# Kernel tuning notes

Measured on AMD Instinct MI355X. Metric: run time of the kernel, lower is better.

The kernel has to match this reference:

```python
import jax, jax.numpy as jnp
import numpy as np

B, S, CACHE, HID, NH, NKV, HD, INTER = 2, 1024, 2048, 2048, 8, 1, 256, 16384
EPS = 1e-6
SOFTCAP = 50.0
SCALE = HD ** -0.5  # query_pre_attn_scalar is None -> head_dim**-0.5
NEG = -1e9


def _rms(x, w, eps=EPS):
    # Gemma RMSNorm: fp32 norm, output scaled by (1 + weight)
    x32 = x.astype(jnp.float32)
    n = x32 * jax.lax.rsqrt(jnp.mean(x32 * x32, axis=-1, keepdims=True) + eps)
    return (n * (1.0 + w)).astype(x.dtype)


def _rope(x, cos, sin):
    # half-split complex rotation (Gemma apply_rotary_emb): first half real, second half imag
    d2 = x.shape[-1] // 2
    x1, x2 = x[..., :d2], x[..., d2:]
    c = cos[None, :, None, :]
    s = sin[None, :, None, :]
    return jnp.concatenate([x1 * c - x2 * s, x1 * s + x2 * c], axis=-1).astype(x.dtype)


def setup_inputs() -> dict:
    key = jax.random.key(0)
    ks = jax.random.split(key, 8)
    sc = lambda k, sh, f: jax.random.normal(k, sh, jnp.float32) * f
    inp = {}
    inp["hidden_states"] = sc(ks[0], (B, S, HID), 1.0)
    inv = 1.0 / (10000.0 ** (np.arange(0, HD, 2, dtype=np.float32) / HD))
    t = np.arange(S, dtype=np.float32)[:, None] * inv[None, :]
    inp["cos"] = jnp.asarray(np.cos(t), jnp.float32)
    inp["sin"] = jnp.asarray(np.sin(t), jnp.float32)
    inp["kv_write_indices"] = jnp.arange(S, dtype=jnp.int32)
    inp["k_cache"] = jnp.zeros((B, CACHE, NKV, HD), jnp.float32)
    inp["v_cache"] = jnp.zeros((B, CACHE, NKV, HD), jnp.float32)
    i = jnp.arange(S)[:, None]
    j = jnp.arange(CACHE)[None, :]
    inp["mask"] = jnp.where(j <= i, 0.0, NEG).astype(jnp.float32)[None, None]  # [1,1,S,CACHE]
    inp["w_qkv"] = sc(ks[1], ((NH + 2 * NKV) * HD, HID), 0.02)
    inp["w_o"] = sc(ks[2], (HID, NH * HD), 0.02)
    inp["w_gate"] = sc(ks[3], (INTER, HID), 0.02)
    inp["w_up"] = sc(ks[4], (INTER, HID), 0.02)
    inp["w_down"] = sc(ks[5], (HID, INTER), 0.02)
    inp["ln_in"] = jnp.zeros((HID,), jnp.float32)
    inp["ln_post"] = jnp.zeros((HID,), jnp.float32)
    inp["q_norm"] = jnp.zeros((HD,), jnp.float32)
    inp["k_norm"] = jnp.zeros((HD,), jnp.float32)
    return inp


def reference(hidden_states, cos, sin, kv_write_indices, k_cache, v_cache, mask,
              w_qkv, w_o, w_gate, w_up, w_down, ln_in, ln_post, q_norm, k_norm):
    # ---- attention sub-block ----
    res = hidden_states
    x = _rms(hidden_states, ln_in)
    qkv = x @ w_qkv.T  # [B,S,(NH+2*NKV)*HD]
    xq, xk, xv = jnp.split(qkv, [NH * HD, NH * HD + NKV * HD], axis=-1)
    xq = xq.reshape(B, S, NH, HD)
    xk = xk.reshape(B, S, NKV, HD)
    xv = xv.reshape(B, S, NKV, HD)
    xq = _rms(xq, q_norm)  # QK-norm
    xk = _rms(xk, k_norm)
    xq = _rope(xq, cos, sin)
    xk = _rope(xk, cos, sin)
    # KV-cache write (index_copy_ on dim 1)
    k_cache = k_cache.at[:, kv_write_indices].set(xk)
    v_cache = v_cache.at[:, kv_write_indices].set(xv)
    key = jnp.repeat(k_cache, NH // NKV, axis=2)  # [B,CACHE,NH,HD]
    val = jnp.repeat(v_cache, NH // NKV, axis=2)
    scores = jnp.einsum('bshd,bthd->bhst', xq * SCALE, key)  # [B,NH,S,CACHE]
    scores = jnp.tanh(scores / SOFTCAP) * SOFTCAP            # logit softcapping
    probs = jax.nn.softmax(scores + mask, axis=-1)
    out = jnp.einsum('bhst,bthd->bshd', probs, val).reshape(B, S, NH * HD)
    h = res + out @ w_o.T
    # ---- MLP sub-block ----
    res = h
    x = _rms(h, ln_post)
    gate = jax.nn.gelu(x @ w_gate.T, approximate=True)
    up = x @ w_up.T
    return res + (gate * up) @ w_down.T
```

## Files before the change

kernel.cpp:

```cpp
#include <hip/hip_runtime.h>
#include <hip/hip_bf16.h>

typedef __attribute__((ext_vector_type(8))) short short8;
typedef __attribute__((ext_vector_type(4))) float f32x4;
typedef unsigned short u16;

#define B_N 2
#define S_N 1024
#define HID_N 2048
#define NH_N 8
#define HD_N 256
#define INTER_N 16384

#define GLB(p) ((const __attribute__((address_space(1))) void*)(p))
#define AS3(p) ((__attribute__((address_space(3))) void*)(p))

__device__ inline u16 f2b_rn(float f) {
    union { float f; unsigned int u; } x; x.f = f;
    unsigned int r = x.u + 0x7fffu + ((x.u >> 16) & 1u);
    return (u16)(r >> 16);
}
__device__ inline float b2f(u16 h) {
    union { unsigned int u; float f; } x; x.u = ((unsigned int)h) << 16;
    return x.f;
}
__device__ inline float gelu_fast(float v) {
    float z = 0.7978845608028654f * (v + 0.044715f * v * v * v);
    float e = exp2f(z * 2.8853900817779268f);
    float th = 1.f - 2.f * __builtin_amdgcn_rcpf(e + 1.f);
    return 0.5f * v * (1.f + th);
}

__global__ __launch_bounds__(256) void convert_f2b(const float* __restrict__ in,
                                                   u16* __restrict__ out, int n4) {
    int i = blockIdx.x * 256 + threadIdx.x;
    int stride = gridDim.x * 256;
    for (; i < n4; i += stride) {
        float4 v = reinterpret_cast<const float4*>(in)[i];
        u16 o[4] = { f2b_rn(v.x), f2b_rn(v.y), f2b_rn(v.z), f2b_rn(v.w) };
        reinterpret_cast<ulonglong1*>(out)[i] = *reinterpret_cast<ulonglong1*>(o);
    }
}

__global__ __launch_bounds__(256) void convert_gu(const float* __restrict__ wg,
                                                  const float* __restrict__ wu,
                                                  u16* __restrict__ out, int n4) {
    int i = blockIdx.x * 256 + threadIdx.x;
    int stride = gridDim.x * 256;
    for (; i < n4; i += stride) {
        const int e = i << 2;
        const int r = e >> 11, c = e & 2047;
        const int rg = ((r >> 7) << 8) + (r & 127);
        float4 g = reinterpret_cast<const float4*>(wg)[i];
        u16 og[4] = { f2b_rn(g.x), f2b_rn(g.y), f2b_rn(g.z), f2b_rn(g.w) };
        *reinterpret_cast<ulonglong1*>(out + (size_t)rg * 2048 + c) =
            *reinterpret_cast<ulonglong1*>(og);
        float4 u = reinterpret_cast<const float4*>(wu)[i];
        u16 ou[4] = { f2b_rn(u.x), f2b_rn(u.y), f2b_rn(u.z), f2b_rn(u.w) };
        *reinterpret_cast<ulonglong1*>(out + (size_t)(rg + 128) * 2048 + c) =
            *reinterpret_cast<ulonglong1*>(ou);
    }
}

__global__ __launch_bounds__(256) void rmsnorm_k(const float* __restrict__ x,
                                                 const float* __restrict__ w,
                                                 u16* __restrict__ out) {
    const int row = blockIdx.x;
    const int tid = threadIdx.x;
    const float* xr = x + (size_t)row * HID_N;
    const float4* xr4 = reinterpret_cast<const float4*>(xr);
    float4 a = xr4[tid * 2], b = xr4[tid * 2 + 1];
    float s = a.x*a.x + a.y*a.y + a.z*a.z + a.w*a.w
            + b.x*b.x + b.y*b.y + b.z*b.z + b.w*b.w;
    for (int off = 32; off > 0; off >>= 1) s += __shfl_xor(s, off, 64);
    __shared__ float red[4];
    if ((tid & 63) == 0) red[tid >> 6] = s;
    __syncthreads();
    float tot = red[0] + red[1] + red[2] + red[3];
    float inv = rsqrtf(tot * (1.0f / HID_N) + 1e-6f);
    const float4* w4 = reinterpret_cast<const float4*>(w);
    float4 wa = w4[tid * 2], wb = w4[tid * 2 + 1];
    short8 o;
    o[0] = (short)f2b_rn(a.x * inv * (1.f + wa.x));
    o[1] = (short)f2b_rn(a.y * inv * (1.f + wa.y));
    o[2] = (short)f2b_rn(a.z * inv * (1.f + wa.z));
    o[3] = (short)f2b_rn(a.w * inv * (1.f + wa.w));
    o[4] = (short)f2b_rn(b.x * inv * (1.f + wb.x));
    o[5] = (short)f2b_rn(b.y * inv * (1.f + wb.y));
    o[6] = (short)f2b_rn(b.z * inv * (1.f + wb.z));
    o[7] = (short)f2b_rn(b.w * inv * (1.f + wb.w));
    reinterpret_cast<short8*>(out + (size_t)row * HID_N)[tid] = o;
}

__global__ __launch_bounds__(256) void qkv_post_k(const float* __restrict__ qkv,
                                                  const float* __restrict__ cosb,
                                                  const float* __restrict__ sinb,
                                                  const int* __restrict__ kvw,
                                                  const float* __restrict__ qn,
                                                  const float* __restrict__ kn,
                                                  u16* __restrict__ qb,
                                                  u16* __restrict__ kb,
                                                  u16* __restrict__ vt) {
    const int bs = blockIdx.x, vi = blockIdx.y;
    const int b = bs >> 10, s = bs & 1023;
    const int tid = threadIdx.x;
    const float* row = qkv + (size_t)bs * 2560;
    const int sdst = kvw[s];
    if (vi == 9) {
        vt[((size_t)(b * 256 + tid)) * 1024 + sdst] = f2b_rn(row[2304 + tid]);
        return;
    }
    __shared__ float buf[256];
    __shared__ float red[4];
    float val = row[vi * 256 + tid];
    float ss = val * val;
    for (int off = 32; off > 0; off >>= 1) ss += __shfl_xor(ss, off, 64);
    if ((tid & 63) == 0) red[tid >> 6] = ss;
    __syncthreads();
    float ms = (red[0] + red[1] + red[2] + red[3]) * (1.f / 256.f) + 1e-6f;
    const float* nw = (vi < 8) ? qn : kn;
    float nrm = val * rsqrtf(ms) * (1.f + nw[tid]);
    buf[tid] = nrm;
    __syncthreads();
    const float cv = cosb[s * 128 + (tid & 127)];
    const float sv = sinb[s * 128 + (tid & 127)];
    float o;
    if (tid < 128) o = buf[tid] * cv - buf[tid + 128] * sv;
    else           o = buf[tid - 128] * sv + buf[tid] * cv;
    if (vi < 8) qb[(((size_t)(b * 8 + vi)) * 1024 + s) * 256 + tid] = f2b_rn(o * 0.0625f);
    else        kb[((size_t)(b * 1024 + sdst)) * 256 + tid] = f2b_rn(o);
}

__global__ __launch_bounds__(256) void attn_k(const u16* __restrict__ qb,
                                              const u16* __restrict__ kb,
                                              const u16* __restrict__ vt,
                                              float* __restrict__ po,
                                              float* __restrict__ pl) {
    const int qt = blockIdx.x;
    const int h  = blockIdx.y;
    const int c  = blockIdx.z >> 1;
    const int b  = blockIdx.z & 1;
    if (qt < 4 * c) return;
    const int tid = threadIdx.x, lane = tid & 63, wid = tid >> 6;
    const int g = lane >> 4, li = lane & 15;
    const int q0 = qt * 64 + wid * 16;
    const int kv_lo = c * 256;
    __shared__ u16 pbuf[4][16 * 32];

    short8 qf[8];
    const size_t qbase = (((size_t)(b * 8 + h)) * 1024 + q0 + li) * 256;
    #pragma unroll
    for (int kk = 0; kk < 8; ++kk)
        qf[kk] = *reinterpret_cast<const short8*>(qb + qbase + kk * 32 + g * 8);

    f32x4 o[16], o1;
    #pragma unroll
    for (int d = 0; d < 16; ++d) o[d] = f32x4{0.f, 0.f, 0.f, 0.f};
    o1 = f32x4{0.f, 0.f, 0.f, 0.f};
    short8 onesf;
    #pragma unroll
    for (int j = 0; j < 8; ++j) onesf[j] = (short)0x3F80;

    const int nt = (min(kv_lo + 256, q0 + 16) - kv_lo + 31) >> 5;
    const int prd = li * 32 + ((g * 8) ^ (((li >> 2) & 3) * 8));

    for (int t = 0; t < nt; ++t) {
        const int kv0 = kv_lo + t * 32;
        f32x4 sc[2];
        sc[0] = f32x4{0.f, 0.f, 0.f, 0.f};
        sc[1] = f32x4{0.f, 0.f, 0.f, 0.f};
        #pragma unroll
        for (int ch = 0; ch < 2; ++ch) {
            const size_t kbase = ((size_t)(b * 1024 + kv0 + ch * 16 + li)) * 256;
            #pragma unroll
            for (int kk = 0; kk < 8; ++kk) {
                short8 kf = *reinterpret_cast<const short8*>(kb + kbase + kk * 32 + g * 8);
                sc[ch] = __builtin_amdgcn_mfma_f32_16x16x32_bf16(qf[kk], kf, sc[ch], 0, 0, 0);
            }
        }
        #pragma unroll
        for (int reg = 0; reg < 4; ++reg) {
            const int qrow = q0 + g * 4 + reg;
            const int prow = g * 4 + reg;
            const int pswz = ((prow >> 2) & 3) * 8;
            #pragma unroll
            for (int ch = 0; ch < 2; ++ch) {
                const int col = kv0 + ch * 16 + li;
                float s = sc[ch][reg];
                float e = exp2f(s * 0.05770780163555854f);
                float th = 1.f - 2.f * __builtin_amdgcn_rcpf(e + 1.f);
                float pv = exp2f(th * 72.13475204444817f);
                pv = (col <= qrow) ? pv : 0.f;
                pbuf[wid][prow * 32 + ((ch * 16 + li) ^ pswz)] = f2b_rn(pv);
            }
        }
        short8 pf = *reinterpret_cast<const short8*>(&pbuf[wid][prd]);
        o1 = __builtin_amdgcn_mfma_f32_16x16x32_bf16(pf, onesf, o1, 0, 0, 0);
        #pragma unroll
        for (int dth = 0; dth < 2; ++dth) {
            short8 vf[8];
            #pragma unroll
            for (int d8 = 0; d8 < 8; ++d8) {
                const int dt = dth * 8 + d8;
                vf[d8] = *reinterpret_cast<const short8*>(
                    vt + ((size_t)(b * 256 + dt * 16 + li)) * 1024 + kv0 + g * 8);
            }
            #pragma unroll
            for (int d8 = 0; d8 < 8; ++d8)
                o[dth * 8 + d8] = __builtin_amdgcn_mfma_f32_16x16x32_bf16(pf, vf[d8], o[dth * 8 + d8], 0, 0, 0);
        }
    }
    const size_t pbase = ((size_t)((c * 2 + b) * 8 + h)) * 1024;
    #pragma unroll
    for (int reg = 0; reg < 4; ++reg) {
        const int row = q0 + g * 4 + reg;
        #pragma unroll
        for (int dt = 0; dt < 16; ++dt)
            po[(pbase + row) * 256 + dt * 16 + li] = o[dt][reg];
        if (li == 0) pl[pbase + row] = o1[reg];
    }
}

__global__ __launch_bounds__(256) void attn_red_k(const float* __restrict__ po,
                                                  const float* __restrict__ pl,
                                                  u16* __restrict__ out) {
    const int gid = blockIdx.x;
    const int b = gid >> 10, s = gid & 1023;
    const int tid = threadIdx.x;
    const int h = tid >> 5, d0 = (tid & 31) * 8;
    const int cmax = s >> 8;
    float l = 0.f;
    float4 a0 = float4{0.f, 0.f, 0.f, 0.f}, a1 = float4{0.f, 0.f, 0.f, 0.f};
    for (int ci = 0; ci <= cmax; ++ci) {
        const size_t r = ((size_t)((ci * 2 + b) * 8 + h)) * 1024 + s;
        l += pl[r];
        float4 b0 = *reinterpret_cast<const float4*>(po + r * 256 + d0);
        float4 b1 = *reinterpret_cast<const float4*>(po + r * 256 + d0 + 4);
        a0.x += b0.x; a0.y += b0.y; a0.z += b0.z; a0.w += b0.w;
        a1.x += b1.x; a1.y += b1.y; a1.z += b1.z; a1.w += b1.w;
    }
    const float inv = 1.f / l;
    u16 r[8] = { f2b_rn(a0.x * inv), f2b_rn(a0.y * inv), f2b_rn(a0.z * inv), f2b_rn(a0.w * inv),
                 f2b_rn(a1.x * inv), f2b_rn(a1.y * inv), f2b_rn(a1.z * inv), f2b_rn(a1.w * inv) };
    *reinterpret_cast<ulonglong2*>(out + ((size_t)gid) * 2048 + h * 256 + d0) =
        *reinterpret_cast<ulonglong2*>(r);
}

template <int EPI>
__global__ __launch_bounds__(256) void gemm_bt(const u16* __restrict__ A,
                                               const u16* __restrict__ W,
                                               const float* __restrict__ res,
                                               float* __restrict__ outf,
                                               int M, int N, int K) {
    __shared__ u16 As[2][128 * 64];
    __shared__ u16 Bs[2][128 * 64];
    const int tid = threadIdx.x, lane = tid & 63, wid = tid >> 6;
    const int g = lane >> 4, li = lane & 15;
    const int wr = wid >> 1, wc = wid & 1;
    const int m0 = blockIdx.x * 128, n0 = blockIdx.y * 128;

    f32x4 acc[4][4];
    #pragma unroll
    for (int m = 0; m < 4; ++m)
        #pragma unroll
        for (int n = 0; n < 4; ++n) acc[m][n] = f32x4{0.f, 0.f, 0.f, 0.f};

    const int lrow = lane >> 3;
    const int lcol = (lane & 7) ^ lrow;
    const u16* ga0 = A + (size_t)(m0 + wid * 32 + lrow) * K + lcol * 8;
    const u16* gb0 = W + (size_t)(n0 + wid * 32 + lrow) * K + lcol * 8;
    const int lbase = wid * 32 * 64;

    auto STAGE = [&](int buf, int k0) {
        #pragma unroll
        for (int i = 0; i < 4; ++i) {
            __builtin_amdgcn_global_load_lds(GLB(ga0 + k0 + (size_t)(i * 8) * K),
                                             AS3(&As[buf][lbase + i * 8 * 64]), 16, 0, 0);
            __builtin_amdgcn_global_load_lds(GLB(gb0 + k0 + (size_t)(i * 8) * K),
                                             AS3(&Bs[buf][lbase + i * 8 * 64]), 16, 0, 0);
        }
    };

    const int NT = K >> 6;
    STAGE(0, 0);
    int cur = 0;
    for (int t = 0; t < NT; ++t) {
        if (t + 1 < NT) {
            STAGE(cur ^ 1, (t + 1) << 6);
            asm volatile("s_waitcnt vmcnt(8)" ::: "memory");
        } else {
            asm volatile("s_waitcnt vmcnt(0)" ::: "memory");
        }
        __builtin_amdgcn_s_barrier();
        __builtin_amdgcn_sched_barrier(0);
        #pragma unroll
        for (int kh = 0; kh < 2; ++kh) {
            short8 af[4], bfr[4];
            #pragma unroll
            for (int m = 0; m < 4; ++m) {
                int rw = wr * 64 + m * 16 + li;
                int slot = (kh * 4 + g) ^ (rw & 7);
                af[m] = *reinterpret_cast<const short8*>(&As[cur][rw * 64 + slot * 8]);
            }
            #pragma unroll
            for (int n = 0; n < 4; ++n) {
                int rw = wc * 64 + n * 16 + li;
                int slot = (kh * 4 + g) ^ (rw & 7);
                bfr[n] = *reinterpret_cast<const short8*>(&Bs[cur][rw * 64 + slot * 8]);
            }
            #pragma unroll
            for (int m = 0; m < 4; ++m)
                #pragma unroll
                for (int n = 0; n < 4; ++n)
                    acc[m][n] = __builtin_amdgcn_mfma_f32_16x16x32_bf16(af[m], bfr[n], acc[m][n], 0, 0, 0);
        }
        __builtin_amdgcn_s_barrier();
        cur ^= 1;
    }

    #pragma unroll
    for (int m = 0; m < 4; ++m) {
        #pragma unroll
        for (int n = 0; n < 4; ++n) {
            #pragma unroll
            for (int reg = 0; reg < 4; ++reg) {
                int row = m0 + wr * 64 + m * 16 + g * 4 + reg;
                int col = n0 + wc * 64 + n * 16 + li;
                size_t idx = (size_t)row * N + col;
                float v = acc[m][n][reg];
                if (EPI == 0) outf[idx] = v;
                else          outf[idx] = v + res[idx];
            }
        }
    }
}

template <int EPI>
__global__ __launch_bounds__(512, 2) void gemm256(const u16* __restrict__ A,
                                                  const u16* __restrict__ W,
                                                  float* __restrict__ outf,
                                                  u16* __restrict__ outb,
                                                  int M, int N, int K, int kcN) {
    __shared__ u16 Als[2][256 * 64];
    __shared__ u16 Bls[2][256 * 64];
    const int tid = threadIdx.x, lane = tid & 63, wid = tid >> 6;
    const int g = lane >> 4, li = lane & 15;
    const int wm = wid >> 2, wn = wid & 3;
    const int m0 = blockIdx.y * 256, n0 = blockIdx.x * 256;

    int koff = 0, Keff = K;
    if (EPI == 4) {
        Keff = K / kcN;
        koff = blockIdx.z * Keff;
        outf += (size_t)blockIdx.z * M * N;
    }

    f32x4 acc[8][4];
    #pragma unroll
    for (int m = 0; m < 8; ++m)
        #pragma unroll
        for (int n = 0; n < 4; ++n) acc[m][n] = f32x4{0.f, 0.f, 0.f, 0.f};

    const int srcg = ((tid & 7) ^ ((tid >> 3) & 7)) * 8;
    const u16* Asrc = A + (size_t)(m0 + (tid >> 3)) * K + koff + srcg;
    const u16* Bsrc = W + (size_t)(n0 + (tid >> 3)) * K + koff + srcg;
    const int dstb = wid * 512;

    auto STAGE_A = [&](int bf, int h, int kt) {
        const int k0 = kt << 6;
        #pragma unroll
        for (int i = 0; i < 2; ++i)
            __builtin_amdgcn_global_load_lds(GLB(Asrc + (size_t)(h * 128 + i * 64) * K + k0),
                                             AS3(&Als[bf][h * 8192 + i * 4096 + dstb]), 16, 0, 0);
    };
    auto STAGE_B = [&](int bf, int h, int kt) {
        const int k0 = kt << 6;
        #pragma unroll
        for (int i = 0; i < 2; ++i)
            __builtin_amdgcn_global_load_lds(GLB(Bsrc + (size_t)(h * 128 + i * 64) * K + k0),
                                             AS3(&Bls[bf][h * 8192 + i * 4096 + dstb]), 16, 0, 0);
    };
    auto LDA = [&](short8* d, int mh, int cb) {
        #pragma unroll
        for (int m = 0; m < 4; ++m) {
            const int rw = mh * 128 + wm * 64 + m * 16 + li;
            #pragma unroll
            for (int kh = 0; kh < 2; ++kh) {
                const int slot = (kh * 4 + g) ^ (rw & 7);
                d[m * 2 + kh] = *reinterpret_cast<const short8*>(&Als[cb][rw * 64 + slot * 8]);
            }
        }
    };
    auto LDB = [&](short8* d, int nh, int cb) {
        #pragma unroll
        for (int n = 0; n < 2; ++n) {
            const int rw = nh * 128 + wn * 32 + n * 16 + li;
            #pragma unroll
            for (int kh = 0; kh < 2; ++kh) {
                const int slot = (kh * 4 + g) ^ (rw & 7);
                d[n * 2 + kh] = *reinterpret_cast<const short8*>(&Bls[cb][rw * 64 + slot * 8]);
            }
        }
    };

    short8 af[8], af2[8], bq0[4], bq1[4];
    auto MQ = [&](int mh, int nh, short8* aa, short8* bb) {
        #pragma unroll
        for (int kh = 0; kh < 2; ++kh)
            #pragma unroll
            for (int m = 0; m < 4; ++m)
                #pragma unroll
                for (int n = 0; n < 2; ++n)
                    acc[mh * 4 + m][nh * 2 + n] = __builtin_amdgcn_mfma_f32_16x16x32_bf16(
                        aa[m * 2 + kh], bb[n * 2 + kh], acc[mh * 4 + m][nh * 2 + n], 0, 0, 0);
    };

    const int NT = Keff >> 6;
    STAGE_A(0, 0, 0); STAGE_B(0, 0, 0); STAGE_B(0, 1, 0); STAGE_A(0, 1, 0);
    {
        const int t1 = (1 < NT) ? 1 : NT - 1;
        STAGE_A(1, 0, t1); STAGE_B(1, 0, t1); STAGE_B(1, 1, t1);
    }
    asm volatile("s_waitcnt vmcnt(6)" ::: "memory");
    __builtin_amdgcn_s_barrier();
    __builtin_amdgcn_sched_barrier(0);
    LDA(af2, 0, 0);

    int cur = 0;
    for (int t = 0; t < NT; ++t) {
        const int tp1 = (t + 1 < NT) ? t + 1 : NT - 1;
        const int tp2 = (t + 2 < NT) ? t + 2 : NT - 1;
        LDB(bq0, 0, cur);
        STAGE_A(cur ^ 1, 1, tp1);
        __builtin_amdgcn_s_barrier();
        __builtin_amdgcn_s_setprio(1);
        MQ(0, 0, af2, bq0);
        __builtin_amdgcn_s_setprio(0);
        __builtin_amdgcn_s_barrier();
        LDB(bq1, 1, cur);
        STAGE_A(cur, 0, tp2);
        __builtin_amdgcn_s_barrier();
        __builtin_amdgcn_s_setprio(1);
        MQ(0, 1, af2, bq1);
        __builtin_amdgcn_s_setprio(0);
        __builtin_amdgcn_s_barrier();
        LDA(af, 1, cur);
        STAGE_B(cur, 0, tp2);
        __builtin_amdgcn_s_barrier();
        __builtin_amdgcn_s_setprio(1);
        MQ(1, 1, af, bq1);
        __builtin_amdgcn_s_setprio(0);
        __builtin_amdgcn_s_barrier();
        STAGE_B(cur, 1, tp2);
        __builtin_amdgcn_s_setprio(1);
        MQ(1, 0, af, bq0);
        __builtin_amdgcn_s_setprio(0);
        asm volatile("s_waitcnt vmcnt(6)" ::: "memory");
        __builtin_amdgcn_s_barrier();
        __builtin_amdgcn_sched_barrier(0);
        LDA(af2, 0, cur ^ 1);
        cur ^= 1;
    }

    if (EPI == 5) {
        #pragma unroll
        for (int mg = 0; mg < 8; ++mg) {
            const int mh = mg >> 2, m = mg & 3;
            #pragma unroll
            for (int n = 0; n < 2; ++n) {
                const int col = (n0 >> 1) + wn * 32 + n * 16 + li;
                #pragma unroll
                for (int reg = 0; reg < 4; ++reg) {
                    const int row = m0 + mh * 128 + wm * 64 + m * 16 + g * 4 + reg;
                    float gt = gelu_fast(acc[mg][n][reg]);
                    float up = acc[mg][n + 2][reg];
                    outb[(size_t)row * INTER_N + col] = f2b_rn(gt * up);
                }
            }
        }
    } else {
        #pragma unroll
        for (int mg = 0; mg < 8; ++mg) {
            const int mh = mg >> 2, m = mg & 3;
            #pragma unroll
            for (int ng = 0; ng < 4; ++ng) {
                const int nh = ng >> 1, n = ng & 1;
                #pragma unroll
                for (int reg = 0; reg < 4; ++reg) {
                    const int row = m0 + mh * 128 + wm * 64 + m * 16 + g * 4 + reg;
                    const int col = n0 + nh * 128 + wn * 32 + n * 16 + li;
                    outf[(size_t)row * N + col] = acc[mg][ng][reg];
                }
            }
        }
    }
}

__global__ __launch_bounds__(256) void reduce4_k(const float* __restrict__ part,
                                                 const float* __restrict__ res,
                                                 float* __restrict__ out, int n4) {
    int i = blockIdx.x * 256 + threadIdx.x;
    int stride = gridDim.x * 256;
    const size_t ps = (size_t)HID_N * B_N * S_N / 4;
    const float4* p4 = reinterpret_cast<const float4*>(part);
    const float4* r4 = reinterpret_cast<const float4*>(res);
    float4* o4 = reinterpret_cast<float4*>(out);
    for (; i < n4; i += stride) {
        float4 a = p4[i], b = p4[i + ps], c = p4[i + 2 * ps], d = p4[i + 3 * ps];
        float4 r = r4[i];
        float4 o;
        o.x = r.x + a.x + b.x + c.x + d.x;
        o.y = r.y + a.y + b.y + c.y + d.y;
        o.z = r.z + a.z + b.z + c.z + d.z;
        o.w = r.w + a.w + b.w + c.w + d.w;
        o4[i] = o;
    }
}

extern "C" void kernel_launch(void* const* d_in, const int* in_sizes, int n_in,
                              void* d_out, int out_size, void* d_ws, size_t ws_size,
                              hipStream_t stream) {
    (void)in_sizes; (void)n_in; (void)out_size; (void)ws_size;
    const float* hs     = (const float*)d_in[0];
    const float* cosb   = (const float*)d_in[1];
    const float* sinb   = (const float*)d_in[2];
    const int*   kvw    = (const int*)d_in[3];
    const float* wqkv   = (const float*)d_in[7];
    const float* wo     = (const float*)d_in[8];
    const float* wg     = (const float*)d_in[9];
    const float* wu     = (const float*)d_in[10];
    const float* wd     = (const float*)d_in[11];
    const float* ln_in  = (const float*)d_in[12];
    const float* ln_post= (const float*)d_in[13];
    const float* qn     = (const float*)d_in[14];
    const float* kn     = (const float*)d_in[15];
    float* out = (float*)d_out;

    char* p = (char*)d_ws;
    auto alloc = [&](size_t bytes) {
        char* r = p;
        p += (bytes + 255) & ~(size_t)255;
        return r;
    };
    u16* wqkv_b = (u16*)alloc(2560ull * 2048 * 2);
    u16* wo_b   = (u16*)alloc(2048ull * 2048 * 2);
    u16* wgu_b  = (u16*)alloc(32768ull * 2048 * 2);
    u16* wd_b   = (u16*)alloc(2048ull * 16384 * 2);
    u16* xn     = (u16*)alloc(2048ull * 2048 * 2);
    float* qkvf = (float*)alloc(2048ull * 2560 * 4);
    u16* qbuf   = (u16*)alloc(2ull * 8 * 1024 * 256 * 2);
    u16* kbuf   = (u16*)alloc(2ull * 1024 * 256 * 2);
    u16* vtbuf  = (u16*)alloc(2ull * 256 * 1024 * 2);
    u16* attn_o = (u16*)alloc(2048ull * 2048 * 2);
    float* hbuf = (float*)alloc(2048ull * 2048 * 4);
    u16* x2     = (u16*)alloc(2048ull * 2048 * 2);
    u16* actb   = (u16*)alloc(2048ull * 16384 * 2);
    float* po   = (float*)alloc(8ull * 8 * 1024 * 256 * 4);
    float* plse = (float*)alloc(8ull * 8 * 1024 * 4);
    float* partials = (float*)d_ws;

    auto conv = [&](const float* src, u16* dst, long n) {
        int n4 = (int)(n / 4);
        long blk = (n4 + 255) / 256;
        if (blk > 4096) blk = 4096;
        convert_f2b<<<dim3((unsigned)blk), dim3(256), 0, stream>>>(src, dst, n4);
    };
    conv(wqkv, wqkv_b, 2560l * 2048);
    conv(wo,   wo_b,   2048l * 2048);
    convert_gu<<<dim3(4096), dim3(256), 0, stream>>>(wg, wu, wgu_b, 8388608);
    conv(wd,   wd_b,   2048l * 16384);

    rmsnorm_k<<<dim3(2048), dim3(256), 0, stream>>>(hs, ln_in, xn);
    gemm_bt<0><<<dim3(16, 20), dim3(256), 0, stream>>>(xn, wqkv_b, nullptr,
                                                       qkvf, 2048, 2560, 2048);
    qkv_post_k<<<dim3(2048, 10), dim3(256), 0, stream>>>(qkvf, cosb, sinb, kvw, qn, kn,
                                                         qbuf, kbuf, vtbuf);
    attn_k<<<dim3(16, 8, 8), dim3(256), 0, stream>>>(qbuf, kbuf, vtbuf, po, plse);
    attn_red_k<<<dim3(2048), dim3(256), 0, stream>>>(po, plse, attn_o);
    gemm_bt<1><<<dim3(16, 16), dim3(256), 0, stream>>>(attn_o, wo_b, hs,
                                                       hbuf, 2048, 2048, 2048);
    rmsnorm_k<<<dim3(2048), dim3(256), 0, stream>>>(hbuf, ln_post, x2);
    gemm256<5><<<dim3(128, 8), dim3(512), 0, stream>>>(x2, wgu_b, nullptr, actb,
                                                       2048, 16384, 2048, 1);
    gemm256<4><<<dim3(8, 8, 4), dim3(512), 0, stream>>>(actb, wd_b, partials, nullptr,
                                                        2048, 2048, 16384, 4);
    reduce4_k<<<dim3(2048), dim3(256), 0, stream>>>(partials, hbuf, out, 1048576);
}
```

Before: 899.3 us.

## Rewrite 256x256 MLP GEMM to 1024-thread blocks with simple double buffering

The 256x256 GEMM used for the gate/up and down projections now runs with 16 waves per block instead of 8. Each wave owns a 64x64 output sub-tile with 16 accumulators instead of 32. The staged half-tile pipeline with setprio and interleaved LDS loads is replaced by a plain double-buffered loop: prefetch the next K-tile, wait, barrier, then compute. The gate/up weight interleave is changed to 32-row groups to match the new per-wave column split in the GELU epilogue. The aim is to cut register pressure and raise the wave count, at the cost of less careful overlap between memory and MFMA work and only one block per CU.

Measured after the change: 811.2 us, median of 3. 1.11x faster.

```diff
diff --git a/kernel.cpp b/kernel.cpp
--- a/kernel.cpp
+++ b/kernel.cpp
@@ -50,14 +50,14 @@
     for (; i < n4; i += stride) {
         const int e = i << 2;
         const int r = e >> 11, c = e & 2047;
-        const int rg = ((r >> 7) << 8) + (r & 127);
+        const int rg = ((r >> 5) << 6) + (r & 31);
         float4 g = reinterpret_cast<const float4*>(wg)[i];
         u16 og[4] = { f2b_rn(g.x), f2b_rn(g.y), f2b_rn(g.z), f2b_rn(g.w) };
         *reinterpret_cast<ulonglong1*>(out + (size_t)rg * 2048 + c) =
             *reinterpret_cast<ulonglong1*>(og);
         float4 u = reinterpret_cast<const float4*>(wu)[i];
         u16 ou[4] = { f2b_rn(u.x), f2b_rn(u.y), f2b_rn(u.z), f2b_rn(u.w) };
-        *reinterpret_cast<ulonglong1*>(out + (size_t)(rg + 128) * 2048 + c) =
+        *reinterpret_cast<ulonglong1*>(out + (size_t)(rg + 32) * 2048 + c) =
             *reinterpret_cast<ulonglong1*>(ou);
     }
 }
@@ -336,11 +336,11 @@
 }
 
 template <int EPI>
-__global__ __launch_bounds__(512, 2) void gemm256(const u16* __restrict__ A,
-                                                  const u16* __restrict__ W,
-                                                  float* __restrict__ outf,
-                                                  u16* __restrict__ outb,
-                                                  int M, int N, int K, int kcN) {
+__global__ __launch_bounds__(1024) void gemm256(const u16* __restrict__ A,
+                                                const u16* __restrict__ W,
+                                                float* __restrict__ outf,
+                                                u16* __restrict__ outb,
+                                                int M, int N, int K, int kcN) {
     __shared__ u16 Als[2][256 * 64];
     __shared__ u16 Bls[2][256 * 64];
     const int tid = threadIdx.x, lane = tid & 63, wid = tid >> 6;
@@ -355,141 +355,91 @@
         outf += (size_t)blockIdx.z * M * N;
     }
 
-    f32x4 acc[8][4];
-    #pragma unroll
-    for (int m = 0; m < 8; ++m)
+    f32x4 acc[4][4];
+    #pragma unroll
+    for (int m = 0; m < 4; ++m)
         #pragma unroll
         for (int n = 0; n < 4; ++n) acc[m][n] = f32x4{0.f, 0.f, 0.f, 0.f};
 
-    const int srcg = ((tid & 7) ^ ((tid >> 3) & 7)) * 8;
-    const u16* Asrc = A + (size_t)(m0 + (tid >> 3)) * K + koff + srcg;
-    const u16* Bsrc = W + (size_t)(n0 + (tid >> 3)) * K + koff + srcg;
+    const int trow = tid >> 3;
+    const int sgr = ((tid & 7) ^ (trow & 7)) * 8;
+    const u16* Asrc = A + (size_t)(m0 + trow) * K + koff + sgr;
+    const u16* Bsrc = W + (size_t)(n0 + trow) * K + koff + sgr;
     const int dstb = wid * 512;
 
-    auto STAGE_A = [&](int bf, int h, int kt) {
+    auto STAGE = [&](int bf, int kt) {
         const int k0 = kt << 6;
         #pragma unroll
-        for (int i = 0; i < 2; ++i)
-            __builtin_amdgcn_global_load_lds(GLB(Asrc + (size_t)(h * 128 + i * 64) * K + k0),
-                                             AS3(&Als[bf][h * 8192 + i * 4096 + dstb]), 16, 0, 0);
+        for (int i = 0; i < 2; ++i) {
+            __builtin_amdgcn_global_load_lds(GLB(Asrc + (size_t)(i * 128) * K + k0),
+                                             AS3(&Als[bf][i * 8192 + dstb]), 16, 0, 0);
+            __builtin_amdgcn_global_load_lds(GLB(Bsrc + (size_t)(i * 128) * K + k0),
+                                             AS3(&Bls[bf][i * 8192 + dstb]), 16, 0, 0);
+        }
     };
-    auto STAGE_B = [&](int bf, int h, int kt) {
-        const int k0 = kt << 6;
-        #pragma unroll
-        for (int i = 0; i < 2; ++i)
-            __builtin_amdgcn_global_load_lds(GLB(Bsrc + (size_t)(h * 128 + i * 64) * K + k0),
-                                             AS3(&Bls[bf][h * 8192 + i * 4096 + dstb]), 16, 0, 0);
-    };
-    auto LDA = [&](short8* d, int mh, int cb) {
-        #pragma unroll
-        for (int m = 0; m < 4; ++m) {
-            const int rw = mh * 128 + wm * 64 + m * 16 + li;
-            #pragma unroll
-            for (int kh = 0; kh < 2; ++kh) {
+
+    const int NT = Keff >> 6;
+    STAGE(0, 0);
+    int cur = 0;
+    for (int t = 0; t < NT; ++t) {
+        if (t + 1 < NT) {
+            STAGE(cur ^ 1, t + 1);
+            asm volatile("s_waitcnt vmcnt(4)" ::: "memory");
+        } else {
+            asm volatile("s_waitcnt vmcnt(0)" ::: "memory");
+        }
+        __builtin_amdgcn_s_barrier();
+        __builtin_amdgcn_sched_barrier(0);
+        #pragma unroll
+        for (int kh = 0; kh < 2; ++kh) {
+            short8 af[4], bfr[4];
+            #pragma unroll
+            for (int m = 0; m < 4; ++m) {
+                const int rw = wm * 64 + m * 16 + li;
                 const int slot = (kh * 4 + g) ^ (rw & 7);
-                d[m * 2 + kh] = *reinterpret_cast<const short8*>(&Als[cb][rw * 64 + slot * 8]);
-            }
-        }
-    };
-    auto LDB = [&](short8* d, int nh, int cb) {
-        #pragma unroll
-        for (int n = 0; n < 2; ++n) {
-            const int rw = nh * 128 + wn * 32 + n * 16 + li;
-            #pragma unroll
-            for (int kh = 0; kh < 2; ++kh) {
+                af[m] = *reinterpret_cast<const short8*>(&Als[cur][rw * 64 + slot * 8]);
+            }
+            #pragma unroll
+            for (int n = 0; n < 4; ++n) {
+                const int rw = wn * 64 + n * 16 + li;
                 const int slot = (kh * 4 + g) ^ (rw & 7);
-                d[n * 2 + kh] = *reinterpret_cast<const short8*>(&Bls[cb][rw * 64 + slot * 8]);
-            }
-        }
-    };
-
-    short8 af[8], af2[8], bq0[4], bq1[4];
-    auto MQ = [&](int mh, int nh, short8* aa, short8* bb) {
-        #pragma unroll
-        for (int kh = 0; kh < 2; ++kh)
+                bfr[n] = *reinterpret_cast<const short8*>(&Bls[cur][rw * 64 + slot * 8]);
+            }
             #pragma unroll
             for (int m = 0; m < 4; ++m)
                 #pragma unroll
-                for (int n = 0; n < 2; ++n)
-                    acc[mh * 4 + m][nh * 2 + n] = __builtin_amdgcn_mfma_f32_16x16x32_bf16(
-                        aa[m * 2 + kh], bb[n * 2 + kh], acc[mh * 4 + m][nh * 2 + n], 0, 0, 0);
-    };
-
-    const int NT = Keff >> 6;
-    STAGE_A(0, 0, 0); STAGE_B(0, 0, 0); STAGE_B(0, 1, 0); STAGE_A(0, 1, 0);
-    {
-        const int t1 = (1 < NT) ? 1 : NT - 1;
-        STAGE_A(1, 0, t1); STAGE_B(1, 0, t1); STAGE_B(1, 1, t1);
-    }
-    asm volatile("s_waitcnt vmcnt(6)" ::: "memory");
-    __builtin_amdgcn_s_barrier();
-    __builtin_amdgcn_sched_barrier(0);
-    LDA(af2, 0, 0);
-
-    int cur = 0;
-    for (int t = 0; t < NT; ++t) {
-        const int tp1 = (t + 1 < NT) ? t + 1 : NT - 1;
-        const int tp2 = (t + 2 < NT) ? t + 2 : NT - 1;
-        LDB(bq0, 0, cur);
-        STAGE_A(cur ^ 1, 1, tp1);
+                for (int n = 0; n < 4; ++n)
+                    acc[m][n] = __builtin_amdgcn_mfma_f32_16x16x32_bf16(af[m], bfr[n], acc[m][n], 0, 0, 0);
+        }
         __builtin_amdgcn_s_barrier();
-        __builtin_amdgcn_s_setprio(1);
-        MQ(0, 0, af2, bq0);
-        __builtin_amdgcn_s_setprio(0);
-        __builtin_amdgcn_s_barrier();
-        LDB(bq1, 1, cur);
-        STAGE_A(cur, 0, tp2);
-        __builtin_amdgcn_s_barrier();
-        __builtin_amdgcn_s_setprio(1);
-        MQ(0, 1, af2, bq1);
-        __builtin_amdgcn_s_setprio(0);
-        __builtin_amdgcn_s_barrier();
-        LDA(af, 1, cur);
-        STAGE_B(cur, 0, tp2);
-        __builtin_amdgcn_s_barrier();
-        __builtin_amdgcn_s_setprio(1);
-        MQ(1, 1, af, bq1);
-        __builtin_amdgcn_s_setprio(0);
-        __builtin_amdgcn_s_barrier();
-        STAGE_B(cur, 1, tp2);
-        __builtin_amdgcn_s_setprio(1);
-        MQ(1, 0, af, bq0);
-        __builtin_amdgcn_s_setprio(0);
-        asm volatile("s_waitcnt vmcnt(6)" ::: "memory");
-        __builtin_amdgcn_s_barrier();
-        __builtin_amdgcn_sched_barrier(0);
-        LDA(af2, 0, cur ^ 1);
         cur ^= 1;
     }
 
     if (EPI == 5) {
         #pragma unroll
-        for (int mg = 0; mg < 8; ++mg) {
-            const int mh = mg >> 2, m = mg & 3;
+        for (int m = 0; m < 4; ++m) {
             #pragma unroll
             for (int n = 0; n < 2; ++n) {
                 const int col = (n0 >> 1) + wn * 32 + n * 16 + li;
                 #pragma unroll
                 for (int reg = 0; reg < 4; ++reg) {
-                    const int row = m0 + mh * 128 + wm * 64 + m * 16 + g * 4 + reg;
-                    float gt = gelu_fast(acc[mg][n][reg]);
-                    float up = acc[mg][n + 2][reg];
+                    const int row = m0 + wm * 64 + m * 16 + g * 4 + reg;
+                    float gt = gelu_fast(acc[m][n][reg]);
+                    float up = acc[m][n + 2][reg];
                     outb[(size_t)row * INTER_N + col] = f2b_rn(gt * up);
                 }
             }
         }
     } else {
         #pragma unroll
-        for (int mg = 0; mg < 8; ++mg) {
-            const int mh = mg >> 2, m = mg & 3;
-            #pragma unroll
-            for (int ng = 0; ng < 4; ++ng) {
-                const int nh = ng >> 1, n = ng & 1;
+        for (int m = 0; m < 4; ++m) {
+            #pragma unroll
+            for (int n = 0; n < 4; ++n) {
                 #pragma unroll
                 for (int reg = 0; reg < 4; ++reg) {
-                    const int row = m0 + mh * 128 + wm * 64 + m * 16 + g * 4 + reg;
-                    const int col = n0 + nh * 128 + wn * 32 + n * 16 + li;
-                    outf[(size_t)row * N + col] = acc[mg][ng][reg];
+                    const int row = m0 + wm * 64 + m * 16 + g * 4 + reg;
+                    const int col = n0 + wn * 64 + n * 16 + li;
+                    outf[(size_t)row * N + col] = acc[m][n][reg];
                 }
             }
         }
@@ -580,9 +530,9 @@
     gemm_bt<1><<<dim3(16, 16), dim3(256), 0, stream>>>(attn_o, wo_b, hs,
                                                        hbuf, 2048, 2048, 2048);
     rmsnorm_k<<<dim3(2048), dim3(256), 0, stream>>>(hbuf, ln_post, x2);
-    gemm256<5><<<dim3(128, 8), dim3(512), 0, stream>>>(x2, wgu_b, nullptr, actb,
-                                                       2048, 16384, 2048, 1);
-    gemm256<4><<<dim3(8, 8, 4), dim3(512), 0, stream>>>(actb, wd_b, partials, nullptr,
-                                                        2048, 2048, 16384, 4);
+    gemm256<5><<<dim3(128, 8), dim3(1024), 0, stream>>>(x2, wgu_b, nullptr, actb,
+                                                        2048, 16384, 2048, 1);
+    gemm256<4><<<dim3(8, 8, 4), dim3(1024), 0, stream>>>(actb, wd_b, partials, nullptr,
+                                                         2048, 2048, 16384, 4);
     reduce4_k<<<dim3(2048), dim3(256), 0, stream>>>(partials, hbuf, out, 1048576);
 }
```
